# Optimization experiments

Measured on AMD Instinct MI355X. Metric: run time of the kernel, lower is better.

Reference implementation:

```python
import math
import jax, jax.numpy as jnp
import numpy as np

HEAD_DIM = 16
# static gather indices for upper triangle (excluding diagonal)
_TRIU_I, _TRIU_J = np.triu_indices(HEAD_DIM, k=1)
_TRIU_I = jnp.asarray(_TRIU_I)
_TRIU_J = jnp.asarray(_TRIU_J)


def setup_inputs() -> dict:
    key = jax.random.key(0)
    x = jax.random.normal(key, (4, 16, 8192, HEAD_DIM), dtype=jnp.float32)
    return {"x": x}


def reference(x):
    d = x.shape[-1]
    rd = math.sqrt(d)        # sqrt(head_dim)
    rrd = math.sqrt(rd)      # head_dim ** 0.25
    r2 = math.sqrt(2.0)
    # outer product z[..., i, j] = x_i * x_j
    z = jnp.einsum('...i,...j->...ij', x, x)
    x2_1 = z[..., _TRIU_I, _TRIU_J]          # upper triangle, excl diag: [..., d(d-1)/2]
    x2_2 = x * x                              # diagonal of outer product: [..., d]
    ones = jnp.ones_like(x[..., 0:1])
    return jnp.concatenate([ones, x / rrd, x2_2 / (rd * r2), x2_1 / rd], axis=-1)
```

## Files before the change

### kernel.cpp

```cpp
#include <hip/hip_runtime.h>

#define D 16
#define OUTD 153
#define ROWS_PER_BLOCK 64
#define THREADS 256

template<int LO, int HI>
__device__ __forceinline__ void emit_cols(const float xv[D], float* dst) {
    if (LO <= 0 && 0 < HI) dst[0] = 1.0f;
#pragma unroll
    for (int k = 0; k < D; ++k) {
        const int c1 = 1 + k;
        if (c1 >= LO && c1 < HI) dst[c1] = xv[k] * 0.5f;
        const int c2 = 17 + k;
        if (c2 >= LO && c2 < HI) dst[c2] = xv[k] * xv[k] * 0.17677669529663687f;
    }
#pragma unroll
    for (int i = 0; i < D; ++i) {
#pragma unroll
        for (int j = i + 1; j < D; ++j) {
            const int c = 33 + (15 * i - (i * (i - 1)) / 2) + (j - i - 1);
            if (c >= LO && c < HI) dst[c] = xv[i] * xv[j] * 0.25f;
        }
    }
}

__global__ __launch_bounds__(THREADS) void taylor_fm_kernel(const float* __restrict__ x,
                                                            float* __restrict__ out,
                                                            int nrows) {
    __shared__ float olds[ROWS_PER_BLOCK * OUTD];
    const int tid = threadIdx.x;
    const int q   = tid >> 6;
    const int r   = tid & 63;
    const int r0  = blockIdx.x * ROWS_PER_BLOCK;
    const int row = r0 + r;

    if (row < nrows) {
        const float4* xrow = reinterpret_cast<const float4*>(x + (size_t)row * D);
        float xv[D];
#pragma unroll
        for (int m = 0; m < 4; ++m) {
            float4 v = xrow[m];
            xv[4 * m + 0] = v.x; xv[4 * m + 1] = v.y;
            xv[4 * m + 2] = v.z; xv[4 * m + 3] = v.w;
        }
        float* dst = olds + r * OUTD;
        if      (q == 0) emit_cols<0,   39 >(xv, dst);
        else if (q == 1) emit_cols<39,  77 >(xv, dst);
        else if (q == 2) emit_cols<77,  115>(xv, dst);
        else             emit_cols<115, 153>(xv, dst);
    }
    __syncthreads();

    const int nrow_blk = min(ROWS_PER_BLOCK, nrows - r0);
    const int nelem = nrow_blk * OUTD;
    const int nf4 = nelem >> 2;
    float4* gout = reinterpret_cast<float4*>(out + (size_t)r0 * OUTD);
    const float4* lsrc = reinterpret_cast<const float4*>(olds);
    for (int g = tid; g < nf4; g += THREADS) gout[g] = lsrc[g];
    const int rem = nelem & 3;
    if (tid < rem) out[(size_t)r0 * OUTD + nf4 * 4 + tid] = olds[nf4 * 4 + tid];
}

extern "C" void kernel_launch(void* const* d_in, const int* in_sizes, int n_in,
                              void* d_out, int out_size, void* d_ws, size_t ws_size,
                              hipStream_t stream) {
    const float* x = (const float*)d_in[0];
    float* out = (float*)d_out;
    const int nrows = in_sizes[0] / D;
    const int blocks = (nrows + ROWS_PER_BLOCK - 1) / ROWS_PER_BLOCK;
    taylor_fm_kernel<<<blocks, THREADS, 0, stream>>>(x, out, nrows);
}
```

Measured before the change: 72.31 us.

## Use persistent grid-stride blocks with register double-buffered input prefetch

Replaces the one-tile-per-block launch with a capped grid of persistent blocks that loop over tiles in a grid-stride pattern. Each iteration prefetches the next tile's input row into a second register buffer while the current tile's shared-memory staging is written out to global memory. This aims to hide input load latency and cut block launch overhead. In exchange it adds an extra barrier per tile, more register use, and fewer resident blocks to hide the latency of the store-heavy write-out.

```diff
diff --git a/kernel.cpp b/kernel.cpp
--- a/kernel.cpp
+++ b/kernel.cpp
@@ -2,8 +2,9 @@
 
 #define D 16
 #define OUTD 153
-#define ROWS_PER_BLOCK 64
+#define TILE_ROWS 64
 #define THREADS 256
+#define NBLOCKS 1024
 
 template<int LO, int HI>
 __device__ __forceinline__ void emit_cols(const float xv[D], float* dst) {
@@ -25,25 +26,28 @@
     }
 }
 
-__global__ __launch_bounds__(THREADS) void taylor_fm_kernel(const float* __restrict__ x,
-                                                            float* __restrict__ out,
-                                                            int nrows) {
-    __shared__ float olds[ROWS_PER_BLOCK * OUTD];
-    const int tid = threadIdx.x;
-    const int q   = tid >> 6;
-    const int r   = tid & 63;
-    const int r0  = blockIdx.x * ROWS_PER_BLOCK;
-    const int row = r0 + r;
-
-    if (row < nrows) {
+__device__ __forceinline__ void load_tile(const float* __restrict__ x, int nrows,
+                                          int t, int ntiles, int r, float (&dstv)[D]) {
+    const int row = t * TILE_ROWS + r;
+    if (t < ntiles && row < nrows) {
         const float4* xrow = reinterpret_cast<const float4*>(x + (size_t)row * D);
-        float xv[D];
 #pragma unroll
         for (int m = 0; m < 4; ++m) {
             float4 v = xrow[m];
-            xv[4 * m + 0] = v.x; xv[4 * m + 1] = v.y;
-            xv[4 * m + 2] = v.z; xv[4 * m + 3] = v.w;
+            dstv[4 * m + 0] = v.x; dstv[4 * m + 1] = v.y;
+            dstv[4 * m + 2] = v.z; dstv[4 * m + 3] = v.w;
         }
+    }
+}
+
+__device__ __forceinline__ void tile_body(const float* __restrict__ x,
+                                          float* __restrict__ out, float* olds,
+                                          int nrows, int ntiles, int t, int tnext,
+                                          int tid, int q, int r,
+                                          const float (&xv)[D], float (&nxv)[D]) {
+    const int r0 = t * TILE_ROWS;
+
+    if (r0 + r < nrows) {
         float* dst = olds + r * OUTD;
         if      (q == 0) emit_cols<0,   39 >(xv, dst);
         else if (q == 1) emit_cols<39,  77 >(xv, dst);
@@ -52,14 +56,42 @@
     }
     __syncthreads();
 
-    const int nrow_blk = min(ROWS_PER_BLOCK, nrows - r0);
+    load_tile(x, nrows, tnext, ntiles, r, nxv);
+
+    const int nrow_blk = min(TILE_ROWS, nrows - r0);
     const int nelem = nrow_blk * OUTD;
     const int nf4 = nelem >> 2;
     float4* gout = reinterpret_cast<float4*>(out + (size_t)r0 * OUTD);
     const float4* lsrc = reinterpret_cast<const float4*>(olds);
     for (int g = tid; g < nf4; g += THREADS) gout[g] = lsrc[g];
-    const int rem = nelem & 3;
-    if (tid < rem) out[(size_t)r0 * OUTD + nf4 * 4 + tid] = olds[nf4 * 4 + tid];
+    if (tid < (nelem & 3)) out[(size_t)r0 * OUTD + nf4 * 4 + tid] = olds[nf4 * 4 + tid];
+
+    asm volatile("" ::: "memory");
+    __builtin_amdgcn_sched_barrier(0);
+    __builtin_amdgcn_s_barrier();
+    __builtin_amdgcn_sched_barrier(0);
+    asm volatile("" ::: "memory");
+}
+
+__global__ __launch_bounds__(THREADS) void taylor_fm_kernel(const float* __restrict__ x,
+                                                            float* __restrict__ out,
+                                                            int nrows) {
+    __shared__ float olds[TILE_ROWS * OUTD];
+    const int tid = threadIdx.x;
+    const int q   = tid >> 6;
+    const int r   = tid & 63;
+    const int ntiles = (nrows + TILE_ROWS - 1) / TILE_ROWS;
+    const int stride = gridDim.x;
+
+    float xva[D], xvb[D];
+    int t = blockIdx.x;
+    load_tile(x, nrows, t, ntiles, r, xva);
+
+    for (; t < ntiles; t += 2 * stride) {
+        tile_body(x, out, olds, nrows, ntiles, t, t + stride, tid, q, r, xva, xvb);
+        if (t + stride < ntiles)
+            tile_body(x, out, olds, nrows, ntiles, t + stride, t + 2 * stride, tid, q, r, xvb, xva);
+    }
 }
 
 extern "C" void kernel_launch(void* const* d_in, const int* in_sizes, int n_in,
@@ -68,6 +100,7 @@
     const float* x = (const float*)d_in[0];
     float* out = (float*)d_out;
     const int nrows = in_sizes[0] / D;
-    const int blocks = (nrows + ROWS_PER_BLOCK - 1) / ROWS_PER_BLOCK;
+    const int ntiles = (nrows + TILE_ROWS - 1) / TILE_ROWS;
+    const int blocks = ntiles < NBLOCKS ? ntiles : NBLOCKS;
     taylor_fm_kernel<<<blocks, THREADS, 0, stream>>>(x, out, nrows);
 }
```

After: 76.71 us. 6.1% more time.

## Compute output columns per lane via wave shuffles, writing directly to global

Applied to the files above, without the earlier changes.

Replaces the LDS-staged design, where each thread computed part of a row into shared memory before a block-wide float4 copy-out, with a wave-level scheme. Each wave loads 4 rows (64 floats) with one coalesced load, and each lane owns up to 3 output columns with precomputed index pairs and scales. Lanes fetch operands with __shfl and write scalar stores straight to global memory. This removes shared memory and __syncthreads, but swaps 16-byte vector stores for per-lane scalar stores into rows of 153 floats, which are not 16-byte aligned, and adds two shuffles per output.

```diff
diff --git a/kernel.cpp b/kernel.cpp
--- a/kernel.cpp
+++ b/kernel.cpp
@@ -2,64 +2,62 @@
 
 #define D 16
 #define OUTD 153
-#define ROWS_PER_BLOCK 64
 #define THREADS 256
+#define GPW 2
 
-template<int LO, int HI>
-__device__ __forceinline__ void emit_cols(const float xv[D], float* dst) {
-    if (LO <= 0 && 0 < HI) dst[0] = 1.0f;
-#pragma unroll
-    for (int k = 0; k < D; ++k) {
-        const int c1 = 1 + k;
-        if (c1 >= LO && c1 < HI) dst[c1] = xv[k] * 0.5f;
-        const int c2 = 17 + k;
-        if (c2 >= LO && c2 < HI) dst[c2] = xv[k] * xv[k] * 0.17677669529663687f;
-    }
-#pragma unroll
-    for (int i = 0; i < D; ++i) {
-#pragma unroll
-        for (int j = i + 1; j < D; ++j) {
-            const int c = 33 + (15 * i - (i * (i - 1)) / 2) + (j - i - 1);
-            if (c >= LO && c < HI) dst[c] = xv[i] * xv[j] * 0.25f;
-        }
-    }
-}
 
 __global__ __launch_bounds__(THREADS) void taylor_fm_kernel(const float* __restrict__ x,
                                                             float* __restrict__ out,
                                                             int nrows) {
-    __shared__ float olds[ROWS_PER_BLOCK * OUTD];
-    const int tid = threadIdx.x;
-    const int q   = tid >> 6;
-    const int r   = tid & 63;
-    const int r0  = blockIdx.x * ROWS_PER_BLOCK;
-    const int row = r0 + r;
+    const int tid  = threadIdx.x;
+    const int lane = tid & 63;
+    const int wid  = tid >> 6;
+    const int ngroups = nrows >> 2;
+    const long long g0 = ((long long)blockIdx.x * 4 + wid) * GPW;
 
-    if (row < nrows) {
-        const float4* xrow = reinterpret_cast<const float4*>(x + (size_t)row * D);
-        float xv[D];
+    int   ii[3], jj[3];
+    float sc[3];
+    bool  quad[3];
+#pragma unroll
+    for (int k = 0; k < 3; ++k) {
+        const int c = k * 64 + lane;
+        int i = 0, j = 0; float s = 0.f; bool q = true;
+        if (c == 0)        { s = 0.f; }
+        else if (c < 17)   { i = c - 1;  s = 0.5f; q = false; }
+        else if (c < 33)   { i = c - 17; j = i; s = 0.17677669529663687f; }
+        else if (c < OUTD) { int t = c - 33; i = 0;
+                             while (t >= 15 - i) { t -= 15 - i; ++i; }
+                             j = i + 1 + t; s = 0.25f; }
+        ii[k] = i; jj[k] = j; sc[k] = s; quad[k] = q;
+    }
+
+    float xv[GPW];
+#pragma unroll
+    for (int g = 0; g < GPW; ++g) {
+        const long long grp = g0 + g;
+        xv[g] = (grp < ngroups) ? x[grp * 64 + lane] : 0.f;
+    }
+
+#pragma unroll
+    for (int g = 0; g < GPW; ++g) {
+        const long long grp = g0 + g;
+        if (grp >= ngroups) break;
+        const float v = xv[g];
 #pragma unroll
         for (int m = 0; m < 4; ++m) {
-            float4 v = xrow[m];
-            xv[4 * m + 0] = v.x; xv[4 * m + 1] = v.y;
-            xv[4 * m + 2] = v.z; xv[4 * m + 3] = v.w;
+            float* orow = out + (grp * 4 + m) * OUTD;
+#pragma unroll
+            for (int k = 0; k < 3; ++k) {
+                const int c = k * 64 + lane;
+                const float a  = __shfl(v, m * 16 + ii[k], 64);
+                const float b  = __shfl(v, m * 16 + jj[k], 64);
+                const float be = quad[k] ? b : 1.0f;
+                float val = a * be * sc[k];
+                if (k == 0 && c == 0) val = 1.0f;
+                if (c < OUTD) orow[c] = val;
+            }
         }
-        float* dst = olds + r * OUTD;
-        if      (q == 0) emit_cols<0,   39 >(xv, dst);
-        else if (q == 1) emit_cols<39,  77 >(xv, dst);
-        else if (q == 2) emit_cols<77,  115>(xv, dst);
-        else             emit_cols<115, 153>(xv, dst);
     }
-    __syncthreads();
-
-    const int nrow_blk = min(ROWS_PER_BLOCK, nrows - r0);
-    const int nelem = nrow_blk * OUTD;
-    const int nf4 = nelem >> 2;
-    float4* gout = reinterpret_cast<float4*>(out + (size_t)r0 * OUTD);
-    const float4* lsrc = reinterpret_cast<const float4*>(olds);
-    for (int g = tid; g < nf4; g += THREADS) gout[g] = lsrc[g];
-    const int rem = nelem & 3;
-    if (tid < rem) out[(size_t)r0 * OUTD + nf4 * 4 + tid] = olds[nf4 * 4 + tid];
 }
 
 extern "C" void kernel_launch(void* const* d_in, const int* in_sizes, int n_in,
@@ -68,6 +66,8 @@
     const float* x = (const float*)d_in[0];
     float* out = (float*)d_out;
     const int nrows = in_sizes[0] / D;
-    const int blocks = (nrows + ROWS_PER_BLOCK - 1) / ROWS_PER_BLOCK;
+    const int ngroups = nrows >> 2;
+    const int waves_needed = (ngroups + GPW - 1) / GPW;
+    const int blocks = (waves_needed + 3) / 4;
     taylor_fm_kernel<<<blocks, THREADS, 0, stream>>>(x, out, nrows);
 }
```

Result: slower. 89.54 us (+23.8%).
